# Kernel tuning notes

Hardware: AMD Instinct MI355X
Metric: run time of the kernel (lower is better)

Reference implementation:

```python
import jax, jax.numpy as jnp
import numpy as np
import math

EPS = 1e-5        # matches module-level EPS used to normalize loc
K_PROP = 16       # proposals per element for Wood's rejection sampler (accept rate >>0.5 for m=5)


def _log_ive_1p5(x):
    """log of exponentially-scaled modified Bessel I_{3/2}(x)*exp(-x), closed form for half-integer order.
    I_{3/2}(x) = sqrt(2/(pi x)) * (cosh(x) - sinh(x)/x);  with the exp(-x) scaling
    cosh(x)e^{-x} = (1+e^{-2x})/2 and sinh(x)e^{-x} = (1-e^{-2x})/2."""
    em2 = jnp.exp(-2.0 * x)
    val = jnp.sqrt(2.0 / (jnp.pi * x)) * ((1.0 + em2) * 0.5 - (1.0 - em2) / (2.0 * x))
    return jnp.log(val)


def _vmf_forward(kappa_mu, n_samples, key):
    B, V, m = kappa_mu.shape            # m = vmf_dim + 1 (must be 5 for the closed-form Bessel)
    scale = jnp.linalg.norm(kappa_mu, axis=2, keepdims=True)     # [B,V,1] = kappa
    loc = kappa_mu / (scale + EPS)                               # [B,V,m] unit mean direction

    # --- Wood's rejection sampling constants (as in hyperspherical_vae VonMisesFisher) ---
    c = jnp.sqrt(4.0 * scale ** 2 + (m - 1) ** 2)
    b_true = (-2.0 * scale + c) / (m - 1)
    b_app = (m - 1) / (4.0 * scale)
    s = jnp.clip(scale - 10.0, 0.0, 1.0)          # smooth switch to Taylor approx for large kappa
    b = b_app * s + b_true * (1.0 - s)
    a = (m - 1 + 2.0 * scale + c) / 4.0
    d = (4.0 * a * b) / (1.0 + b) - (m - 1) * math.log(m - 1)

    kb, ku, kv = jax.random.split(key, 3)
    con = (m - 1) / 2.0
    prop_shape = (n_samples, B, V, 1, K_PROP)
    e = jax.random.beta(kb, con, con, prop_shape)                          # Beta proposals
    u = jax.random.uniform(ku, prop_shape, minval=1e-20, maxval=1.0 - 1e-20)
    bb = b[None, ..., None]
    aa = a[None, ..., None]
    dd = d[None, ..., None]
    denom = 1.0 - (1.0 - bb) * e
    w_prop = (1.0 - (1.0 + bb) * e) / denom
    t = (2.0 * aa * bb) / denom
    accept = ((m - 1.0) * jnp.log(t) - t + dd) > jnp.log(u)               # [n,B,V,1,K]
    idx = jnp.argmax(accept, axis=-1)                                      # first accepted proposal
    w = jnp.take_along_axis(w_prop, idx[..., None], axis=-1)[..., 0]       # [n,B,V,1]

    # --- tangent direction + concatenate to sphere point ---
    v = jax.random.normal(kv, (n_samples, B, V, m - 1))
    v = v / jnp.linalg.norm(v, axis=-1, keepdims=True)
    w_ = jnp.sqrt(jnp.clip(1.0 - w ** 2, 1e-10))
    x = jnp.concatenate([w, w_ * v], axis=-1)                              # [n,B,V,m]

    # --- Householder rotation mapping e1 -> loc ---
    e1 = jnp.zeros((m,), dtype=kappa_mu.dtype).at[0].set(1.0)
    uvec = e1 - loc
    uvec = uvec / (jnp.linalg.norm(uvec, axis=-1, keepdims=True) + 1e-5)
    z = x - 2.0 * jnp.sum(x * uvec, axis=-1, keepdims=True) * uvec         # [n,B,V,m]

    # --- log prob under each vMF, summed over the product factors ---
    sc = scale[..., 0]                                                     # [B,V]
    log_unnorm = jnp.sum(loc * z, axis=-1) * sc                            # [n,B,V]
    log_norm = -((m / 2 - 1) * jnp.log(sc) - (m / 2) * math.log(2 * math.pi)
                 - (sc + _log_ive_1p5(sc)))                                 # [B,V]
    log_prob = jnp.sum(log_unnorm - log_norm, axis=-1)                     # [n,B]

    samples = z.reshape(n_samples, B, V * m)                               # [n,B,z_dim]
    return samples.transpose(1, 0, 2), log_prob.transpose(1, 0)            # [B,n,z_dim], [B,n]


def setup_inputs() -> dict:
    key = jax.random.key(0)
    B, V, m = 2048, 64, 5
    kappa_mu = jax.random.normal(key, (B, V, m), dtype=jnp.float32)
    return {"kappa_mu": kappa_mu, "n_samples": 16}


def reference(kappa_mu, n_samples):
    key = jax.random.key(1)
    samples, log_prob = _vmf_forward(kappa_mu, n_samples, key)
    return samples, log_prob
```

## Files before the change

kernel.cpp:

```cpp
#include <hip/hip_runtime.h>
#include <stdint.h>
#include <math.h>

#pragma clang fp contract(off)

struct U2 { uint32_t x, y; };

__host__ __device__ constexpr U2 tf(uint32_t k0, uint32_t k1, uint32_t x0, uint32_t x1) {
  uint32_t k2 = k0 ^ k1 ^ 0x1BD11BDAu;
#define TF_R(r) { x0 += x1; x1 = (x1 << (r)) | (x1 >> (32 - (r))); x1 ^= x0; }
  x0 += k0; x1 += k1;
  TF_R(13) TF_R(15) TF_R(26) TF_R(6)
  x0 += k1; x1 += k2 + 1u;
  TF_R(17) TF_R(29) TF_R(16) TF_R(24)
  x0 += k2; x1 += k0 + 2u;
  TF_R(13) TF_R(15) TF_R(26) TF_R(6)
  x0 += k0; x1 += k1 + 3u;
  TF_R(17) TF_R(29) TF_R(16) TF_R(24)
  x0 += k1; x1 += k2 + 4u;
  TF_R(13) TF_R(15) TF_R(26) TF_R(6)
  x0 += k2; x1 += k0 + 5u;
#undef TF_R
  return U2{x0, x1};
}

__device__ constexpr U2 T0 = tf(0u, 1u, 0u, 0u);
__device__ constexpr U2 T1 = tf(0u, 1u, 0u, 1u);
__device__ constexpr U2 T2 = tf(0u, 1u, 0u, 2u);
__device__ constexpr U2 KA = tf(T0.x, T0.y, 0u, 0u);
__device__ constexpr U2 KB = tf(T0.x, T0.y, 0u, 1u);

__device__ __forceinline__ U2 srow(U2 k, uint32_t i) { return tf(k.x, k.y, 0u, i); }
__device__ __forceinline__ uint32_t rb(U2 k, uint32_t i) {
  U2 r = tf(k.x, k.y, 0u, i); return r.x ^ r.y;
}

__device__ __forceinline__ float u01f(uint32_t b) {
  return __uint_as_float((b >> 9) | 0x3F800000u) - 1.0f;
}

__device__ float log_x(float a) {
  if (a == 0.0f) return -__builtin_inff();
  if (a < 0.0f) return __builtin_nanf("");
  if (__builtin_isinf(a)) return a;
  uint32_t bits = __float_as_uint(a);
  int e = (int)(bits >> 23) - 126;
  float m = __uint_as_float((bits & 0x007FFFFFu) | 0x3F000000u);
  if (m < 0.70710678118654752440f) { e -= 1; m = m + m - 1.0f; }
  else                             { m = m - 1.0f; }
  float z = m * m;
  float y = fmaf(7.0376836292E-2f, m, -1.1514610310E-1f);
  y = fmaf(y, m,  1.1676998740E-1f);
  y = fmaf(y, m, -1.2420140846E-1f);
  y = fmaf(y, m,  1.4249322787E-1f);
  y = fmaf(y, m, -1.6668057665E-1f);
  y = fmaf(y, m,  2.0000714765E-1f);
  y = fmaf(y, m, -2.4999993993E-1f);
  y = fmaf(y, m,  3.3333331174E-1f);
  y = y * m; y = y * z;
  y = fmaf((float)e, -2.12194440e-4f, y);
  y = fmaf(z, -0.5f, y);
  float r = m + y;
  r = fmaf((float)e, 0.693359375f, r);
  return r;
}

__device__ float exp_x(float a) {
  float x = fminf(a, 88.3762626647950f);
  x = fmaxf(x, -88.3762626647949f);
  float fx = floorf(fmaf(x, 1.44269504088896341f, 0.5f));
  x = x - fx * 0.693359375f;
  x = x - fx * (-2.12194440e-4f);
  float z = x * x;
  float y = fmaf(1.9875691500E-4f, x, 1.3981999507E-3f);
  y = fmaf(y, x, 8.3334519073E-3f);
  y = fmaf(y, x, 4.1665795894E-2f);
  y = fmaf(y, x, 1.6666665459E-1f);
  y = fmaf(y, x, 5.0000001201E-1f);
  y = fmaf(y, z, x);
  y = y + 1.0f;
  return ldexpf(y, (int)fx);
}

__device__ __forceinline__ float log1p_x(float x) {
  float u = 1.0f + x;
  if (u == 1.0f) return x;
  return x * (log_x(u) / (u - 1.0f));
}

__device__ float erfinv_x(float x) {
  float w = -log1p_x(-(x * x));
  float p;
  if (w < 5.0f) {
    w = w - 2.5f;
    p = 2.81022636e-08f;
    p = p * w + 3.43273939e-07f;
    p = p * w + (-3.5233877e-06f);
    p = p * w + (-4.39150654e-06f);
    p = p * w + 0.00021858087f;
    p = p * w + (-0.00125372503f);
    p = p * w + (-0.00417768164f);
    p = p * w + 0.246640727f;
    p = p * w + 1.50140941f;
  } else {
    w = sqrtf(w) - 3.0f;
    p = -0.000200214257f;
    p = p * w + 0.000100950558f;
    p = p * w + 0.00134934322f;
    p = p * w + (-0.00367342844f);
    p = p * w + 0.00573950773f;
    p = p * w + (-0.0076224613f);
    p = p * w + 0.00943887047f;
    p = p * w + 1.00167406f;
    p = p * w + 2.83297682f;
  }
  return p * x;
}

#define F_NEG_ALMOST1 (-0.99999994039535522f)
#define F_SQRT2       (1.4142135623730951f)

#define NB   2048
#define NS   16
#define NV   64
#define ZDIM 320
#define SAMPLES_ELEMS (2048ull*16ull*320ull)
#define NSITES (2048u*16u*64u)
#define NROW   (2048u*64u)
#define CHUNK  256u
#define N_WAVES (NSITES / CHUNK)
#define KEY_OFF (NROW * 3u)
#define WS_FLOATS_NEEDED (KEY_OFF + NSITES * 4u)

__global__ __launch_bounds__(256) void prep_fused(const float* __restrict__ km,
                                                  float* __restrict__ ws,
                                                  float* __restrict__ out,
                                                  int use_ws) {
  uint32_t site = blockIdx.x * 256u + threadIdx.x;
  if (site < NROW) {
    const float* kp = km + (size_t)site * 5u;
    float m0 = kp[0], m1 = kp[1], m2 = kp[2], m3 = kp[3], m4 = kp[4];
    float kap = sqrtf(m0*m0 + m1*m1 + m2*m2 + m3*m3 + m4*m4);
    float cwv = sqrtf(4.0f * (kap * kap) + 16.0f);
    float b_true = (-2.0f * kap + cwv) / 4.0f;
    float b_app  = 4.0f / (4.0f * kap);
    float ssw = fminf(fmaxf(kap - 10.0f, 0.0f), 1.0f);
    float bw = b_app * ssw + b_true * (1.0f - ssw);
    float aw = (4.0f + 2.0f * kap + cwv) / 4.0f;
    float dw = (4.0f * aw * bw) / (1.0f + bw) - 5.545177444479562f;
    ws[site * 3u + 0u] = bw;
    ws[site * 3u + 1u] = aw;
    ws[site * 3u + 2u] = dw;
  }
  uint32_t i = site * 16u;
  U2 kA0 = srow(srow(KA, i), 0u);
  U2 kB0 = srow(srow(KB, i), 0u);
  if (use_ws) {
    float* kt = ws + KEY_OFF + (size_t)site * 4u;
    kt[0] = __uint_as_float(kA0.x);
    kt[1] = __uint_as_float(kA0.y);
    kt[2] = __uint_as_float(kB0.x);
    kt[3] = __uint_as_float(kB0.y);
  } else {
    uint32_t vv = site & (NV - 1u);
    uint32_t sb = site >> 6;
    uint32_t s  = sb >> 11;
    uint32_t b  = sb & (NB - 1u);
    float* zo = out + (size_t)(b * NS + s) * ZDIM + (size_t)vv * 5u;
    zo[1] = __uint_as_float(kA0.x);
    zo[2] = __uint_as_float(kA0.y);
    zo[3] = __uint_as_float(kB0.x);
    zo[4] = __uint_as_float(kB0.y);
  }
}

__global__ __launch_bounds__(256) void sample_w(const float* __restrict__ ws,
                                                float* __restrict__ out,
                                                int use_ws) {
  const int lane = threadIdx.x & 63;
  const uint32_t wave_id = blockIdx.x * 4u + (threadIdx.x >> 6);
  const uint32_t base = wave_id * CHUNK;

  const float Dg = 2.0f - 0.33333334f;
  const float Cg = 0.33333334f * (1.0f / sqrtf(Dg));
  const float logDg = log_x(Dg);
  const unsigned long long lmask_lt = (1ull << lane) - 1ull;

  uint32_t next = 0;
  bool need_site = true;
  bool lane_done = false;
  bool have = false;

  uint32_t site = 0, i = 0;
  int kprop = 0;
  bool phaseB = false;
  U2 k = {0u, 0u};
  U2 kB0 = {0u, 0u};
  float bw = 0.f, aw = 0.f, dw = 0.f, w0 = 0.f, lga = 0.f;
  float* zo_cur = out;

  #pragma unroll 1
  for (int it = 0; it < 20000; ++it) {
    unsigned long long need = __ballot(need_site);
    if (need) {
      if (need_site) {
        uint32_t idx = next + (uint32_t)__popcll(need & lmask_lt);
        if (idx < CHUNK) {
          site = base + idx;
          uint32_t row = site & (NB * NV - 1u);
          bw = ws[row * 3u + 0u];
          aw = ws[row * 3u + 1u];
          dw = ws[row * 3u + 2u];
          uint32_t vv = site & (NV - 1u);
          uint32_t sb = site >> 6;
          uint32_t s  = sb >> 11;
          uint32_t b  = sb & (NB - 1u);
          zo_cur = out + (size_t)(b * NS + s) * ZDIM + (size_t)vv * 5u;
          i = site * 16u;
          kprop = 0; phaseB = false;
          if (use_ws) {
            const float* kt = ws + KEY_OFF + (size_t)site * 4u;
            k.x   = __float_as_uint(kt[0]);
            k.y   = __float_as_uint(kt[1]);
            kB0.x = __float_as_uint(kt[2]);
            kB0.y = __float_as_uint(kt[3]);
          } else {
            k.x   = __float_as_uint(zo_cur[1]);
            k.y   = __float_as_uint(zo_cur[2]);
            kB0.x = __float_as_uint(zo_cur[3]);
            kB0.y = __float_as_uint(zo_cur[4]);
          }
          have = true;
        } else {
          lane_done = true;
          have = false;
        }
        need_site = false;
      }
      next += (uint32_t)__popcll(need);
    }
    if (__all(lane_done)) break;

    if (have) {
      U2 xk = srow(k, 1u);
      U2 Uk = srow(k, 2u);
      U2 sub = srow(xk, 1u);
      float f = u01f(rb(sub, 0u));
      float un = fmaxf(F_NEG_ALMOST1, f * 2.0f + F_NEG_ALMOST1);
      float x = F_SQRT2 * erfinv_x(un);
      float v = 1.0f + x * Cg;
      if (v <= 0.0f) {
        U2 chain = srow(xk, 0u);
        #pragma unroll 1
        for (int r = 0; r < 16 && v <= 0.0f; ++r) {
          U2 sk = srow(chain, 1u);
          chain = srow(chain, 0u);
          float f2 = u01f(rb(sk, 0u));
          float un2 = fmaxf(F_NEG_ALMOST1, f2 * 2.0f + F_NEG_ALMOST1);
          x = F_SQRT2 * erfinv_x(un2);
          v = 1.0f + x * Cg;
        }
      }
      float X = x * x;
      float V = (v * v) * v;
      float lV = log_x(V);
      float U = u01f(rb(Uk, 0u));
      bool c1 = U >= (1.0f - 0.0331f * (X * X));
      bool c2 = log_x(U) >= (X * 0.5f + Dg * ((1.0f - V) + lV));
      if (c1 && c2) {
        k = srow(k, 0u);
      } else {
        float lg = logDg + lV;
        bool finish = false;
        float wres = 0.0f;
        if (!phaseB) {
          lga = lg;
          phaseB = true;
          k = (kprop == 0) ? kB0 : srow(srow(KB, i), 0u);
        } else {
          float lgb = lg;
          bool age = (lga >= lgb);
          float dmin = (age ? lgb : lga) - (age ? lga : lgb);
          float eo = exp_x(dmin);
          float ea = age ? 1.0f : eo;
          float eb = age ? eo : 1.0f;
          float e = ea / (ea + eb);
          float fu = u01f(rb(T1, i));
          float uu = fmaxf(1e-20f, fu * 1.0f + 1e-20f);
          float denom = 1.0f - (1.0f - bw) * e;
          float wp = (1.0f - (1.0f + bw) * e) / denom;
          float tt = (2.0f * aw * bw) / denom;
          float st = 4.0f * log_x(tt) - tt + dw;
          bool acc = st > log_x(uu);
          if (kprop == 0) w0 = wp;
          if (acc) { wres = wp; finish = true; }
          else {
            ++kprop;
            if (kprop == 16) { wres = w0; finish = true; }
            else { ++i; phaseB = false; k = srow(srow(KA, i), 0u); }
          }
        }
        if (finish) {
          zo_cur[0] = wres;
          have = false;
          need_site = true;
        }
      }
    }
  }
}

__global__ __launch_bounds__(256) void vmf_finish(const float* __restrict__ km,
                                                  float* __restrict__ out) {
  const int tid  = threadIdx.x;
  const int wd   = tid >> 6;
  const int lane = tid & 63;
  const int bs   = blockIdx.x * 4 + wd;
  const int b    = bs >> 4;
  const int s    = bs & 15;
  const int vv   = lane;

  const float* kp = km + ((size_t)b * NV + vv) * 5;
  float m0 = kp[0], m1 = kp[1], m2 = kp[2], m3 = kp[3], m4 = kp[4];
  float kap = sqrtf(m0*m0 + m1*m1 + m2*m2 + m3*m3 + m4*m4);
  float l0 = m0 / (kap + 1e-5f);
  float l1 = m1 / (kap + 1e-5f);
  float l2 = m2 / (kap + 1e-5f);
  float l3 = m3 / (kap + 1e-5f);
  float l4 = m4 / (kap + 1e-5f);

  float* zo = out + (size_t)(b * NS + s) * ZDIM + (size_t)vv * 5;
  float w = zo[0];

  const uint32_t site = ((uint32_t)(s * NB + b) * NV + (uint32_t)vv);
  uint32_t j0 = site * 4u;
  float f, un, n0, n1, n2, n3;
  f = u01f(rb(T2, j0 + 0u)); un = fmaxf(F_NEG_ALMOST1, f*2.0f + F_NEG_ALMOST1); n0 = F_SQRT2*erfinv_x(un);
  f = u01f(rb(T2, j0 + 1u)); un = fmaxf(F_NEG_ALMOST1, f*2.0f + F_NEG_ALMOST1); n1 = F_SQRT2*erfinv_x(un);
  f = u01f(rb(T2, j0 + 2u)); un = fmaxf(F_NEG_ALMOST1, f*2.0f + F_NEG_ALMOST1); n2 = F_SQRT2*erfinv_x(un);
  f = u01f(rb(T2, j0 + 3u)); un = fmaxf(F_NEG_ALMOST1, f*2.0f + F_NEG_ALMOST1); n3 = F_SQRT2*erfinv_x(un);
  float nn = sqrtf(n0*n0 + n1*n1 + n2*n2 + n3*n3);
  n0 /= nn; n1 /= nn; n2 /= nn; n3 /= nn;

  float w_ = sqrtf(fmaxf(1.0f - w * w, 1e-10f));
  float x0 = w, x1 = w_ * n0, x2 = w_ * n1, x3 = w_ * n2, x4 = w_ * n3;

  float u0 = 1.0f - l0, u1 = -l1, u2 = -l2, u3 = -l3, u4 = -l4;
  float un_ = sqrtf(u0*u0 + u1*u1 + u2*u2 + u3*u3 + u4*u4);
  u0 /= (un_ + 1e-5f); u1 /= (un_ + 1e-5f); u2 /= (un_ + 1e-5f);
  u3 /= (un_ + 1e-5f); u4 /= (un_ + 1e-5f);
  float dot = x0*u0 + x1*u1 + x2*u2 + x3*u3 + x4*u4;
  float z0 = x0 - (2.0f * dot) * u0;
  float z1 = x1 - (2.0f * dot) * u1;
  float z2 = x2 - (2.0f * dot) * u2;
  float z3 = x3 - (2.0f * dot) * u3;
  float z4 = x4 - (2.0f * dot) * u4;

  zo[0] = z0; zo[1] = z1; zo[2] = z2; zo[3] = z3; zo[4] = z4;

  float dlz = l0*z0 + l1*z1 + l2*z2 + l3*z3 + l4*z4;
  float lu = dlz * kap;
  float em2 = exp_x(-2.0f * kap);
  float val = sqrtf(2.0f / (3.14159274f * kap)) *
              ((1.0f + em2) * 0.5f - (1.0f - em2) / (2.0f * kap));
  float li = log_x(val);
  float term = lu + ((1.5f * log_x(kap) - 4.594692666023363f) - (kap + li));

  float acc = term;
  #pragma unroll
  for (int off = 1; off < 64; off <<= 1) acc += __shfl_xor(acc, off, 64);
  if (lane == 0) out[SAMPLES_ELEMS + (size_t)(b * NS + s)] = acc;
}

extern "C" void kernel_launch(void* const* d_in, const int* in_sizes, int n_in,
                              void* d_out, int out_size, void* d_ws, size_t ws_size,
                              hipStream_t stream) {
  const float* km = (const float*)d_in[0];
  float* out = (float*)d_out;
  float* ws = (float*)d_ws;
  int use_ws = (ws_size >= (size_t)WS_FLOATS_NEEDED * 4u) ? 1 : 0;
  hipLaunchKernelGGL(prep_fused, dim3(NSITES / 256), dim3(256), 0, stream, km, ws, out, use_ws);
  hipLaunchKernelGGL(sample_w,   dim3(N_WAVES / 4),  dim3(256), 0, stream, ws, out, use_ws);
  hipLaunchKernelGGL(vmf_finish, dim3(32768 / 4),    dim3(256), 0, stream, km, out);
}
```

Before: 205.2 us.

## Fuse rejection sampler and finish kernel, passing w through LDS

Merges the sample_w and vmf_finish kernels into one launch. Each wave now stores its accepted w values in shared memory and then does the tangent sampling, Householder reflection and log-prob reduction for the four (s,b) rows its chunk covers. This removes a kernel launch and the global write and re-read of w. The finish work now runs inside the more divergent sampler waves, and the LDS buffer sized by CHUNK may lower occupancy.

```diff
diff --git a/kernel.cpp b/kernel.cpp
--- a/kernel.cpp
+++ b/kernel.cpp
@@ -174,11 +174,14 @@
   }
 }
 
-__global__ __launch_bounds__(256) void sample_w(const float* __restrict__ ws,
-                                                float* __restrict__ out,
-                                                int use_ws) {
+__global__ __launch_bounds__(256) void vmf_fused(const float* __restrict__ km,
+                                                 const float* __restrict__ ws,
+                                                 float* __restrict__ out,
+                                                 int use_ws) {
+  __shared__ float ldsW[4][CHUNK];
   const int lane = threadIdx.x & 63;
-  const uint32_t wave_id = blockIdx.x * 4u + (threadIdx.x >> 6);
+  const int wd   = threadIdx.x >> 6;
+  const uint32_t wave_id = blockIdx.x * 4u + (uint32_t)wd;
   const uint32_t base = wave_id * CHUNK;
 
   const float Dg = 2.0f - 0.33333334f;
@@ -191,13 +194,13 @@
   bool lane_done = false;
   bool have = false;
 
-  uint32_t site = 0, i = 0;
+  uint32_t site = 0, i = 0, idx_cur = 0;
   int kprop = 0;
   bool phaseB = false;
   U2 k = {0u, 0u};
   U2 kB0 = {0u, 0u};
   float bw = 0.f, aw = 0.f, dw = 0.f, w0 = 0.f, lga = 0.f;
-  float* zo_cur = out;
+  const float* kslots = out;
 
   #pragma unroll 1
   for (int it = 0; it < 20000; ++it) {
@@ -207,15 +210,11 @@
         uint32_t idx = next + (uint32_t)__popcll(need & lmask_lt);
         if (idx < CHUNK) {
           site = base + idx;
+          idx_cur = idx;
           uint32_t row = site & (NB * NV - 1u);
           bw = ws[row * 3u + 0u];
           aw = ws[row * 3u + 1u];
           dw = ws[row * 3u + 2u];
-          uint32_t vv = site & (NV - 1u);
-          uint32_t sb = site >> 6;
-          uint32_t s  = sb >> 11;
-          uint32_t b  = sb & (NB - 1u);
-          zo_cur = out + (size_t)(b * NS + s) * ZDIM + (size_t)vv * 5u;
           i = site * 16u;
           kprop = 0; phaseB = false;
           if (use_ws) {
@@ -225,10 +224,15 @@
             kB0.x = __float_as_uint(kt[2]);
             kB0.y = __float_as_uint(kt[3]);
           } else {
-            k.x   = __float_as_uint(zo_cur[1]);
-            k.y   = __float_as_uint(zo_cur[2]);
-            kB0.x = __float_as_uint(zo_cur[3]);
-            kB0.y = __float_as_uint(zo_cur[4]);
+            uint32_t vv = site & (NV - 1u);
+            uint32_t sb = site >> 6;
+            uint32_t s  = sb >> 11;
+            uint32_t b  = sb & (NB - 1u);
+            const float* zo = kslots + (size_t)(b * NS + s) * ZDIM + (size_t)vv * 5u;
+            k.x   = __float_as_uint(zo[1]);
+            k.y   = __float_as_uint(zo[2]);
+            kB0.x = __float_as_uint(zo[3]);
+            kB0.y = __float_as_uint(zo[4]);
           }
           have = true;
         } else {
@@ -301,75 +305,72 @@
           }
         }
         if (finish) {
-          zo_cur[0] = wres;
+          ldsW[wd][idx_cur] = wres;
           have = false;
           need_site = true;
         }
       }
     }
   }
-}
-
-__global__ __launch_bounds__(256) void vmf_finish(const float* __restrict__ km,
-                                                  float* __restrict__ out) {
-  const int tid  = threadIdx.x;
-  const int wd   = tid >> 6;
-  const int lane = tid & 63;
-  const int bs   = blockIdx.x * 4 + wd;
-  const int b    = bs >> 4;
-  const int s    = bs & 15;
-  const int vv   = lane;
-
-  const float* kp = km + ((size_t)b * NV + vv) * 5;
-  float m0 = kp[0], m1 = kp[1], m2 = kp[2], m3 = kp[3], m4 = kp[4];
-  float kap = sqrtf(m0*m0 + m1*m1 + m2*m2 + m3*m3 + m4*m4);
-  float l0 = m0 / (kap + 1e-5f);
-  float l1 = m1 / (kap + 1e-5f);
-  float l2 = m2 / (kap + 1e-5f);
-  float l3 = m3 / (kap + 1e-5f);
-  float l4 = m4 / (kap + 1e-5f);
-
-  float* zo = out + (size_t)(b * NS + s) * ZDIM + (size_t)vv * 5;
-  float w = zo[0];
-
-  const uint32_t site = ((uint32_t)(s * NB + b) * NV + (uint32_t)vv);
-  uint32_t j0 = site * 4u;
-  float f, un, n0, n1, n2, n3;
-  f = u01f(rb(T2, j0 + 0u)); un = fmaxf(F_NEG_ALMOST1, f*2.0f + F_NEG_ALMOST1); n0 = F_SQRT2*erfinv_x(un);
-  f = u01f(rb(T2, j0 + 1u)); un = fmaxf(F_NEG_ALMOST1, f*2.0f + F_NEG_ALMOST1); n1 = F_SQRT2*erfinv_x(un);
-  f = u01f(rb(T2, j0 + 2u)); un = fmaxf(F_NEG_ALMOST1, f*2.0f + F_NEG_ALMOST1); n2 = F_SQRT2*erfinv_x(un);
-  f = u01f(rb(T2, j0 + 3u)); un = fmaxf(F_NEG_ALMOST1, f*2.0f + F_NEG_ALMOST1); n3 = F_SQRT2*erfinv_x(un);
-  float nn = sqrtf(n0*n0 + n1*n1 + n2*n2 + n3*n3);
-  n0 /= nn; n1 /= nn; n2 /= nn; n3 /= nn;
-
-  float w_ = sqrtf(fmaxf(1.0f - w * w, 1e-10f));
-  float x0 = w, x1 = w_ * n0, x2 = w_ * n1, x3 = w_ * n2, x4 = w_ * n3;
-
-  float u0 = 1.0f - l0, u1 = -l1, u2 = -l2, u3 = -l3, u4 = -l4;
-  float un_ = sqrtf(u0*u0 + u1*u1 + u2*u2 + u3*u3 + u4*u4);
-  u0 /= (un_ + 1e-5f); u1 /= (un_ + 1e-5f); u2 /= (un_ + 1e-5f);
-  u3 /= (un_ + 1e-5f); u4 /= (un_ + 1e-5f);
-  float dot = x0*u0 + x1*u1 + x2*u2 + x3*u3 + x4*u4;
-  float z0 = x0 - (2.0f * dot) * u0;
-  float z1 = x1 - (2.0f * dot) * u1;
-  float z2 = x2 - (2.0f * dot) * u2;
-  float z3 = x3 - (2.0f * dot) * u3;
-  float z4 = x4 - (2.0f * dot) * u4;
-
-  zo[0] = z0; zo[1] = z1; zo[2] = z2; zo[3] = z3; zo[4] = z4;
-
-  float dlz = l0*z0 + l1*z1 + l2*z2 + l3*z3 + l4*z4;
-  float lu = dlz * kap;
-  float em2 = exp_x(-2.0f * kap);
-  float val = sqrtf(2.0f / (3.14159274f * kap)) *
-              ((1.0f + em2) * 0.5f - (1.0f - em2) / (2.0f * kap));
-  float li = log_x(val);
-  float term = lu + ((1.5f * log_x(kap) - 4.594692666023363f) - (kap + li));
-
-  float acc = term;
-  #pragma unroll
-  for (int off = 1; off < 64; off <<= 1) acc += __shfl_xor(acc, off, 64);
-  if (lane == 0) out[SAMPLES_ELEMS + (size_t)(b * NS + s)] = acc;
+
+  #pragma unroll 1
+  for (int q = 0; q < 4; ++q) {
+    uint32_t sb = wave_id * 4u + (uint32_t)q;
+    uint32_t s  = sb >> 11;
+    uint32_t b  = sb & (NB - 1u);
+    int vv = lane;
+
+    const float* kp = km + ((size_t)b * NV + vv) * 5;
+    float m0 = kp[0], m1 = kp[1], m2 = kp[2], m3 = kp[3], m4 = kp[4];
+    float kap = sqrtf(m0*m0 + m1*m1 + m2*m2 + m3*m3 + m4*m4);
+    float l0 = m0 / (kap + 1e-5f);
+    float l1 = m1 / (kap + 1e-5f);
+    float l2 = m2 / (kap + 1e-5f);
+    float l3 = m3 / (kap + 1e-5f);
+    float l4 = m4 / (kap + 1e-5f);
+
+    float w = ldsW[wd][q * 64 + lane];
+
+    const uint32_t site_f = sb * NV + (uint32_t)vv;
+    uint32_t j0 = site_f * 4u;
+    float f, un, n0, n1, n2, n3;
+    f = u01f(rb(T2, j0 + 0u)); un = fmaxf(F_NEG_ALMOST1, f*2.0f + F_NEG_ALMOST1); n0 = F_SQRT2*erfinv_x(un);
+    f = u01f(rb(T2, j0 + 1u)); un = fmaxf(F_NEG_ALMOST1, f*2.0f + F_NEG_ALMOST1); n1 = F_SQRT2*erfinv_x(un);
+    f = u01f(rb(T2, j0 + 2u)); un = fmaxf(F_NEG_ALMOST1, f*2.0f + F_NEG_ALMOST1); n2 = F_SQRT2*erfinv_x(un);
+    f = u01f(rb(T2, j0 + 3u)); un = fmaxf(F_NEG_ALMOST1, f*2.0f + F_NEG_ALMOST1); n3 = F_SQRT2*erfinv_x(un);
+    float nn = sqrtf(n0*n0 + n1*n1 + n2*n2 + n3*n3);
+    n0 /= nn; n1 /= nn; n2 /= nn; n3 /= nn;
+
+    float w_ = sqrtf(fmaxf(1.0f - w * w, 1e-10f));
+    float x0 = w, x1 = w_ * n0, x2 = w_ * n1, x3 = w_ * n2, x4 = w_ * n3;
+
+    float u0 = 1.0f - l0, u1 = -l1, u2 = -l2, u3 = -l3, u4 = -l4;
+    float un_ = sqrtf(u0*u0 + u1*u1 + u2*u2 + u3*u3 + u4*u4);
+    u0 /= (un_ + 1e-5f); u1 /= (un_ + 1e-5f); u2 /= (un_ + 1e-5f);
+    u3 /= (un_ + 1e-5f); u4 /= (un_ + 1e-5f);
+    float dot = x0*u0 + x1*u1 + x2*u2 + x3*u3 + x4*u4;
+    float z0 = x0 - (2.0f * dot) * u0;
+    float z1 = x1 - (2.0f * dot) * u1;
+    float z2 = x2 - (2.0f * dot) * u2;
+    float z3 = x3 - (2.0f * dot) * u3;
+    float z4 = x4 - (2.0f * dot) * u4;
+
+    float* zo = out + (size_t)(b * NS + s) * ZDIM + (size_t)vv * 5;
+    zo[0] = z0; zo[1] = z1; zo[2] = z2; zo[3] = z3; zo[4] = z4;
+
+    float dlz = l0*z0 + l1*z1 + l2*z2 + l3*z3 + l4*z4;
+    float lu = dlz * kap;
+    float em2 = exp_x(-2.0f * kap);
+    float val = sqrtf(2.0f / (3.14159274f * kap)) *
+                ((1.0f + em2) * 0.5f - (1.0f - em2) / (2.0f * kap));
+    float li = log_x(val);
+    float term = lu + ((1.5f * log_x(kap) - 4.594692666023363f) - (kap + li));
+
+    float acc = term;
+    #pragma unroll
+    for (int off = 1; off < 64; off <<= 1) acc += __shfl_xor(acc, off, 64);
+    if (lane == 0) out[SAMPLES_ELEMS + (size_t)(b * NS + s)] = acc;
+  }
 }
 
 extern "C" void kernel_launch(void* const* d_in, const int* in_sizes, int n_in,
@@ -380,6 +381,5 @@
   float* ws = (float*)d_ws;
   int use_ws = (ws_size >= (size_t)WS_FLOATS_NEEDED * 4u) ? 1 : 0;
   hipLaunchKernelGGL(prep_fused, dim3(NSITES / 256), dim3(256), 0, stream, km, ws, out, use_ws);
-  hipLaunchKernelGGL(sample_w,   dim3(N_WAVES / 4),  dim3(256), 0, stream, ws, out, use_ws);
-  hipLaunchKernelGGL(vmf_finish, dim3(32768 / 4),    dim3(256), 0, stream, km, out);
-}
+  hipLaunchKernelGGL(vmf_fused,  dim3(N_WAVES / 4),  dim3(256), 0, stream, km, ws, out, use_ws);
+}
```

Result: no change. 204.5 us (-0.3%).
